# Kernel tuning notes

Measured on AMD Instinct MI355X. Metric: run time of the kernel, lower is better.

Reference implementation:

```python
import jax, jax.numpy as jnp
import numpy as np

N_NODES = 200000
N_EDGES = 6400000
D_IN, D_HID, D_OUT = 128, 16, 172


def gcn_conv(x, edge_index, W, b, n):
    """PyG GCNConv: add self-loops, symmetric D^-1/2 A D^-1/2 normalization,
    linear projection, scatter-add aggregation, bias."""
    src, dst = edge_index[0], edge_index[1]
    loops = jnp.arange(n, dtype=edge_index.dtype)
    src = jnp.concatenate([src, loops])
    dst = jnp.concatenate([dst, loops])
    # in-degree with self-loops (>= 1, so rsqrt is safe)
    deg = jax.ops.segment_sum(jnp.ones_like(dst, dtype=x.dtype), dst, num_segments=n)
    dinv = jax.lax.rsqrt(deg)
    lin = x @ W  # [n, d_out]
    norm = dinv[src] * dinv[dst]  # per-edge normalization
    msg = lin[src] * norm[:, None]  # gather + scale
    out = jax.ops.segment_sum(msg, dst, num_segments=n)  # scatter-add
    return out + b


def setup_inputs() -> dict:
    key = jax.random.key(0)
    k1, k2, k3, k4, k5, k6 = jax.random.split(key, 6)
    x = jax.random.normal(k1, (N_NODES, D_IN), dtype=jnp.float32)
    edge_index = jax.random.randint(k2, (2, N_EDGES), 0, N_NODES, dtype=jnp.int64)
    W1 = jax.random.normal(k3, (D_IN, D_HID), dtype=jnp.float32) * (1.0 / np.sqrt(D_IN))
    b1 = jnp.zeros((D_HID,), dtype=jnp.float32)
    W2 = jax.random.normal(k4, (D_HID, D_OUT), dtype=jnp.float32) * (1.0 / np.sqrt(D_HID))
    b2 = jnp.zeros((D_OUT,), dtype=jnp.float32)
    return {"x": x, "edge_index": edge_index, "W1": W1, "b1": b1, "W2": W2, "b2": b2}


def reference(x, edge_index, W1, b1, W2, b2):
    n = x.shape[0]
    # CRD: GCNConv -> relu (dropout is identity in eval mode)
    h = jax.nn.relu(gcn_conv(x, edge_index, W1, b1, n))
    # CLS: GCNConv -> log_softmax over classes
    logits = gcn_conv(h, edge_index, W2, b2, n)
    return jax.nn.log_softmax(logits, axis=1)
```

## Files before the change

kernel.cpp:

```cpp
#include <hip/hip_runtime.h>
#include <hip/hip_fp16.h>

#define N_NODES 200000
#define N_EDGES 6400000
#define D_IN    128
#define D_HID   16
#define D_OUT   172

#define NS1     800
#define EPB     8000
#define SBN     782
#define SB_NODES 256

#define O_BTOT  0
#define O_BASE  1024
#define O_CNT1  2048
#define O_COL   2048
#define O_ROW   6402048
#define O_DINV  6602112
#define O_PACK  6802112
#define O_F16A  6802112
#define O_F16B  8402112
#define O_AGG2  10002112

__global__ __launch_bounds__(256) void k_hist1(const int* __restrict__ dst,
                                               unsigned* __restrict__ counts) {
    __shared__ unsigned cnt[SBN];
    for (int i = threadIdx.x; i < SBN; i += 256) cnt[i] = 0;
    __syncthreads();
    const int* dp = dst + blockIdx.x * EPB;
    for (int i = threadIdx.x; i < EPB; i += 256)
        atomicAdd(&cnt[dp[i] >> 8], 1u);
    __syncthreads();
    unsigned* out = counts + (size_t)blockIdx.x * SBN;
    for (int i = threadIdx.x; i < SBN; i += 256) out[i] = cnt[i];
}

__global__ __launch_bounds__(256) void k_scan_col(unsigned* __restrict__ counts,
                                                  unsigned* __restrict__ btot) {
    __shared__ unsigned arr[NS1];
    int b = blockIdx.x;
    for (int i = threadIdx.x; i < NS1; i += 256)
        arr[i] = counts[(size_t)i * SBN + b];
    __syncthreads();
    if (threadIdx.x < 64) {
        int l = threadIdx.x;
        int lo = l * 13, hi = min(lo + 13, NS1);
        unsigned sum = 0;
        for (int i = lo; i < hi; ++i) sum += arr[i];
        unsigned incl = sum;
#pragma unroll
        for (int o = 1; o < 64; o <<= 1) {
            unsigned tmp = __shfl_up(incl, o);
            if (l >= o) incl += tmp;
        }
        if (l == 63) btot[b] = incl;
        unsigned run = incl - sum;
        for (int i = lo; i < hi; ++i) { unsigned v = arr[i]; arr[i] = run; run += v; }
    }
    __syncthreads();
    for (int i = threadIdx.x; i < NS1; i += 256)
        counts[(size_t)i * SBN + b] = arr[i];
}

__global__ __launch_bounds__(64) void k_scan_base(const unsigned* __restrict__ btot,
                                                  unsigned* __restrict__ base) {
    int l = threadIdx.x;
    int lo = l * 13, hi = min(lo + 13, SBN);
    unsigned sum = 0;
    for (int i = lo; i < hi; ++i) sum += btot[i];
    unsigned incl = sum;
#pragma unroll
    for (int o = 1; o < 64; o <<= 1) {
        unsigned tmp = __shfl_up(incl, o);
        if (l >= o) incl += tmp;
    }
    unsigned run = incl - sum;
    for (int i = lo; i < hi; ++i) { unsigned v = btot[i]; base[i] = run; run += v; }
    if (l == 63) base[SBN] = incl;
}

__global__ __launch_bounds__(256) void k_scatter1(const int* __restrict__ src,
                                                  const int* __restrict__ dst,
                                                  const unsigned* __restrict__ counts,
                                                  const unsigned* __restrict__ base,
                                                  unsigned* __restrict__ packed) {
    __shared__ unsigned off[SBN];
    const unsigned* crow = counts + (size_t)blockIdx.x * SBN;
    for (int i = threadIdx.x; i < SBN; i += 256) off[i] = base[i] + crow[i];
    __syncthreads();
    const int* sp = src + blockIdx.x * EPB;
    const int* dp = dst + blockIdx.x * EPB;
    for (int i = threadIdx.x; i < EPB; i += 256) {
        int s = sp[i], d = dp[i];
        unsigned slot = atomicAdd(&off[d >> 8], 1u);
        packed[slot] = ((unsigned)(d & (SB_NODES - 1)) << 18) | (unsigned)s;
    }
}

__global__ __launch_bounds__(256) void k_csr(const unsigned* __restrict__ packed,
                                             const unsigned* __restrict__ base,
                                             int* __restrict__ rowptr,
                                             float* __restrict__ dinv,
                                             int* __restrict__ col) {
    __shared__ unsigned cnt[SB_NODES];
    __shared__ unsigned off[SB_NODES];
    __shared__ unsigned wsum[4];
    int t = threadIdx.x, sb = blockIdx.x;
    unsigned beg = base[sb], end = base[sb + 1];
    cnt[t] = 0;
    __syncthreads();
    for (unsigned i = beg + t; i < end; i += 256)
        atomicAdd(&cnt[packed[i] >> 18], 1u);
    __syncthreads();
    unsigned e = cnt[t];
    int lane = t & 63, wid = t >> 6;
    unsigned incl = e;
#pragma unroll
    for (int o = 1; o < 64; o <<= 1) {
        unsigned tmp = __shfl_up(incl, o);
        if (lane >= o) incl += tmp;
    }
    if (lane == 63) wsum[wid] = incl;
    __syncthreads();
    unsigned wbase = 0;
    for (int w = 0; w < wid; ++w) wbase += wsum[w];
    unsigned ex = wbase + incl - e;
    off[t] = ex;
    int n0 = sb * SB_NODES + t;
    if (n0 <= N_NODES) rowptr[n0] = (int)(beg + ex);
    if (n0 <  N_NODES) dinv[n0]   = rsqrtf((float)(e + 1));
    __syncthreads();
    for (unsigned i = beg + t; i < end; i += 256) {
        unsigned p = packed[i];
        unsigned slot = atomicAdd(&off[p >> 18], 1u);
        col[beg + slot] = (int)(p & 0x3FFFFu);
    }
}

__global__ __launch_bounds__(256) void k_lin1(const float* __restrict__ x,
                                              const float* __restrict__ W1,
                                              const float* __restrict__ dinv,
                                              __half* __restrict__ lin) {
    __shared__ float sW[D_IN * D_HID];
    for (int t = threadIdx.x; t < D_IN * D_HID; t += 256) sW[t] = W1[t];
    __syncthreads();

    int g  = threadIdx.x & 3;
    int nl = threadIdx.x >> 2;
    int n  = blockIdx.x * 64 + nl;

    float acc[16];
#pragma unroll
    for (int j = 0; j < 16; ++j) acc[j] = 0.f;

    const float4* xr = (const float4*)(x + (size_t)n * D_IN + g * 32);
#pragma unroll
    for (int i = 0; i < 8; ++i) {
        float4 xv = xr[i];
        int k = g * 32 + i * 4;
#pragma unroll
        for (int j = 0; j < 16; ++j) {
            acc[j] += xv.x * sW[(k + 0) * 16 + j] + xv.y * sW[(k + 1) * 16 + j]
                    + xv.z * sW[(k + 2) * 16 + j] + xv.w * sW[(k + 3) * 16 + j];
        }
    }
#pragma unroll
    for (int j = 0; j < 16; ++j) {
        acc[j] += __shfl_xor(acc[j], 1);
        acc[j] += __shfl_xor(acc[j], 2);
    }
    float di = dinv[n];
    ushort4 pk;
    pk.x = __half_as_ushort(__float2half(acc[g * 4 + 0] * di));
    pk.y = __half_as_ushort(__float2half(acc[g * 4 + 1] * di));
    pk.z = __half_as_ushort(__float2half(acc[g * 4 + 2] * di));
    pk.w = __half_as_ushort(__float2half(acc[g * 4 + 3] * di));
    *(ushort4*)(lin + (size_t)n * 16 + g * 4) = pk;
}

template <int MODE>
__global__ __launch_bounds__(256) void k_gather(const int* __restrict__ rowptr,
                                                const int* __restrict__ col,
                                                const float* __restrict__ dinv,
                                                const __half* __restrict__ fin,
                                                const float* __restrict__ bias,
                                                void* __restrict__ outv) {
    int t = threadIdx.x;
    int n = blockIdx.x * 16 + (t >> 4);
    int lane = t & 15;
    int beg = rowptr[n], end = rowptr[n + 1];
    float a0 = __half2float(fin[n * 16 + lane]);
    float a1 = 0.f, a2 = 0.f, a3 = 0.f, a4 = 0.f, a5 = 0.f, a6 = 0.f, a7 = 0.f;
    int i = beg;
    for (; i + 8 <= end; i += 8) {
        int s0 = col[i + 0], s1 = col[i + 1], s2 = col[i + 2], s3 = col[i + 3];
        int s4 = col[i + 4], s5 = col[i + 5], s6 = col[i + 6], s7 = col[i + 7];
        float f0 = __half2float(fin[s0 * 16 + lane]);
        float f1 = __half2float(fin[s1 * 16 + lane]);
        float f2 = __half2float(fin[s2 * 16 + lane]);
        float f3 = __half2float(fin[s3 * 16 + lane]);
        float f4 = __half2float(fin[s4 * 16 + lane]);
        float f5 = __half2float(fin[s5 * 16 + lane]);
        float f6 = __half2float(fin[s6 * 16 + lane]);
        float f7 = __half2float(fin[s7 * 16 + lane]);
        a0 += f0; a1 += f1; a2 += f2; a3 += f3;
        a4 += f4; a5 += f5; a6 += f6; a7 += f7;
    }
    for (; i < end; ++i) a0 += __half2float(fin[col[i] * 16 + lane]);
    float acc = ((a0 + a1) + (a2 + a3)) + ((a4 + a5) + (a6 + a7));
    float dd = dinv[n];
    float v = acc * dd;
    if (MODE) {
        v = fmaxf(v + bias[lane], 0.f) * dd;
        ((__half*)outv)[n * 16 + lane] = __float2half(v);
    } else {
        ((float*)outv)[n * 16 + lane] = v;
    }
}

__global__ __launch_bounds__(256) void k_out(const float* __restrict__ agg2,
                                             const float* __restrict__ W2,
                                             const float* __restrict__ b2,
                                             float* __restrict__ out) {
    __shared__ float sWt[D_OUT * D_HID];
    __shared__ float sb[D_OUT];
    __shared__ float sl[64 * D_OUT];
    __shared__ float sls[64];
    int t = threadIdx.x;
    for (int m = t; m < D_OUT * D_HID; m += 256)
        sWt[m] = W2[(m & 15) * D_OUT + (m >> 4)];
    for (int m = t; m < D_OUT; m += 256) sb[m] = b2[m];
    __syncthreads();

    int nl = t >> 2, q = t & 3;
    int n  = blockIdx.x * 64 + nl;
    const float4* ar = (const float4*)(agg2 + (size_t)n * 16);
    float4 a0 = ar[0], a1 = ar[1], a2 = ar[2], a3 = ar[3];
    float a[16] = {a0.x, a0.y, a0.z, a0.w, a1.x, a1.y, a1.z, a1.w,
                   a2.x, a2.y, a2.z, a2.w, a3.x, a3.y, a3.z, a3.w};

    float mloc = -INFINITY;
    float* srow = sl + nl * D_OUT;
#pragma unroll 4
    for (int i = 0; i < 43; ++i) {
        int c = q + 4 * i;
        const float4* wr = (const float4*)(sWt + c * 16);
        float4 w0 = wr[0], w1 = wr[1], w2 = wr[2], w3 = wr[3];
        float l = sb[c];
        l += a[0]  * w0.x + a[1]  * w0.y + a[2]  * w0.z + a[3]  * w0.w;
        l += a[4]  * w1.x + a[5]  * w1.y + a[6]  * w1.z + a[7]  * w1.w;
        l += a[8]  * w2.x + a[9]  * w2.y + a[10] * w2.z + a[11] * w2.w;
        l += a[12] * w3.x + a[13] * w3.y + a[14] * w3.z + a[15] * w3.w;
        srow[c] = l;
        mloc = fmaxf(mloc, l);
    }
    mloc = fmaxf(mloc, __shfl_xor(mloc, 1));
    mloc = fmaxf(mloc, __shfl_xor(mloc, 2));
    float sloc = 0.f;
#pragma unroll 4
    for (int i = 0; i < 43; ++i) sloc += __expf(srow[q + 4 * i] - mloc);
    sloc += __shfl_xor(sloc, 1);
    sloc += __shfl_xor(sloc, 2);
    if (q == 0) sls[nl] = mloc + __logf(sloc);
    __syncthreads();

    const float4* sl4 = (const float4*)sl;
    float4* ob = (float4*)(out + (size_t)blockIdx.x * 64 * D_OUT);
    for (int jj = t; jj < 64 * D_OUT / 4; jj += 256) {
        float4 v = sl4[jj];
        float ls = sls[jj / 43];
        v.x -= ls; v.y -= ls; v.z -= ls; v.w -= ls;
        ob[jj] = v;
    }
}

extern "C" void kernel_launch(void* const* d_in, const int* in_sizes, int n_in,
                              void* d_out, int out_size, void* d_ws, size_t ws_size,
                              hipStream_t stream) {
    const float* x     = (const float*)d_in[0];
    const int*   edges = (const int*)d_in[1];
    const float* W1    = (const float*)d_in[2];
    const float* b1    = (const float*)d_in[3];
    const float* W2    = (const float*)d_in[4];
    const float* b2    = (const float*)d_in[5];
    float*       out   = (float*)d_out;

    const int* src = edges;
    const int* dst = edges + N_EDGES;

    unsigned* ws     = (unsigned*)d_ws;
    unsigned* btot   = ws + O_BTOT;
    unsigned* base   = ws + O_BASE;
    unsigned* counts = ws + O_CNT1;
    int*      col    = (int*)(ws + O_COL);
    int*      rowptr = (int*)(ws + O_ROW);
    float*    dinv   = (float*)(ws + O_DINV);
    unsigned* packed = ws + O_PACK;
    __half*   f16a   = (__half*)(ws + O_F16A);
    __half*   f16b   = (__half*)(ws + O_F16B);
    float*    agg2   = (float*)(ws + O_AGG2);

    k_hist1    <<<NS1, 256, 0, stream>>>(dst, counts);
    k_scan_col <<<SBN, 256, 0, stream>>>(counts, btot);
    k_scan_base<<<1,    64, 0, stream>>>(btot, base);
    k_scatter1 <<<NS1, 256, 0, stream>>>(src, dst, counts, base, packed);
    k_csr      <<<SBN, 256, 0, stream>>>(packed, base, rowptr, dinv, col);

    k_lin1     <<<N_NODES / 64, 256, 0, stream>>>(x, W1, dinv, f16a);
    k_gather<1><<<N_NODES / 16, 256, 0, stream>>>(rowptr, col, dinv, f16a, b1, f16b);

    k_gather<0><<<N_NODES / 16, 256, 0, stream>>>(rowptr, col, dinv, f16b, b1, agg2);
    k_out      <<<N_NODES / 64, 256, 0, stream>>>(agg2, W2, b2, out);
}
```

Before: 487.9 us.

## Quantize gathered node features to int8 and stage scatter through LDS

Adds per-tensor absmax tracking and an int8 quantization pass so both neighbor-aggregation gathers read 1-byte features with integer accumulation instead of fp16, halving random gather traffic. The scatter into coarse buckets is also restaged in shared memory with a local prefix sum so global writes are contiguous per bucket. This adds two quantize kernels and atomics, and int8 with a single global scale loses considerable precision, which risks tolerance failures.

```diff
diff --git a/kernel.cpp b/kernel.cpp
--- a/kernel.cpp
+++ b/kernel.cpp
@@ -14,14 +14,17 @@
 
 #define O_BTOT  0
 #define O_BASE  1024
-#define O_CNT1  2048
-#define O_COL   2048
-#define O_ROW   6402048
-#define O_DINV  6602112
-#define O_PACK  6802112
-#define O_F16A  6802112
-#define O_F16B  8402112
-#define O_AGG2  10002112
+#define O_SMAX  2048
+#define O_CNT1  2112
+#define O_COL   2112
+#define O_ROW   6402112
+#define O_DINV  6602176
+#define O_PACK  6802176
+#define O_F16A  6802176
+#define O_Q8A   8402176
+#define O_F16B  9202176
+#define O_Q8B   10802176
+#define O_AGG2  6802176
 
 __global__ __launch_bounds__(256) void k_hist1(const int* __restrict__ dst,
                                                unsigned* __restrict__ counts) {
@@ -64,8 +67,10 @@
 }
 
 __global__ __launch_bounds__(64) void k_scan_base(const unsigned* __restrict__ btot,
-                                                  unsigned* __restrict__ base) {
+                                                  unsigned* __restrict__ base,
+                                                  unsigned* __restrict__ smax) {
     int l = threadIdx.x;
+    if (l < 2) smax[l] = 0;
     int lo = l * 13, hi = min(lo + 13, SBN);
     unsigned sum = 0;
     for (int i = lo; i < hi; ++i) sum += btot[i];
@@ -85,16 +90,55 @@
                                                   const unsigned* __restrict__ counts,
                                                   const unsigned* __restrict__ base,
                                                   unsigned* __restrict__ packed) {
+    __shared__ unsigned       sdat[EPB];
+    __shared__ unsigned short sbkt[EPB];
+    __shared__ unsigned cnt[SBN];
     __shared__ unsigned off[SBN];
+    __shared__ unsigned gbs[SBN];
+    __shared__ unsigned wsum[4];
+    int t = threadIdx.x;
     const unsigned* crow = counts + (size_t)blockIdx.x * SBN;
-    for (int i = threadIdx.x; i < SBN; i += 256) off[i] = base[i] + crow[i];
+    for (int i = t; i < SBN; i += 256) { cnt[i] = 0; gbs[i] = base[i] + crow[i]; }
     __syncthreads();
     const int* sp = src + blockIdx.x * EPB;
     const int* dp = dst + blockIdx.x * EPB;
-    for (int i = threadIdx.x; i < EPB; i += 256) {
+    for (int i = t; i < EPB; i += 256) atomicAdd(&cnt[dp[i] >> 8], 1u);
+    __syncthreads();
+    int lane = t & 63, wid = t >> 6;
+    int b0 = t * 4;
+    unsigned c0v = (b0 + 0 < SBN) ? cnt[b0 + 0] : 0;
+    unsigned c1v = (b0 + 1 < SBN) ? cnt[b0 + 1] : 0;
+    unsigned c2v = (b0 + 2 < SBN) ? cnt[b0 + 2] : 0;
+    unsigned c3v = (b0 + 3 < SBN) ? cnt[b0 + 3] : 0;
+    unsigned mysum = c0v + c1v + c2v + c3v;
+    unsigned incl = mysum;
+#pragma unroll
+    for (int o = 1; o < 64; o <<= 1) {
+        unsigned tmp = __shfl_up(incl, o);
+        if (lane >= o) incl += tmp;
+    }
+    if (lane == 63) wsum[wid] = incl;
+    __syncthreads();
+    unsigned wbase = 0;
+    for (int w = 0; w < wid; ++w) wbase += wsum[w];
+    unsigned run = wbase + incl - mysum;
+    if (b0 + 0 < SBN) { off[b0 + 0] = run; run += c0v; }
+    if (b0 + 1 < SBN) { off[b0 + 1] = run; run += c1v; }
+    if (b0 + 2 < SBN) { off[b0 + 2] = run; run += c2v; }
+    if (b0 + 3 < SBN) { off[b0 + 3] = run; run += c3v; }
+    __syncthreads();
+    for (int i = t; i < EPB; i += 256) {
         int s = sp[i], d = dp[i];
-        unsigned slot = atomicAdd(&off[d >> 8], 1u);
-        packed[slot] = ((unsigned)(d & (SB_NODES - 1)) << 18) | (unsigned)s;
+        unsigned b = (unsigned)d >> 8;
+        unsigned slot = atomicAdd(&off[b], 1u);
+        sdat[slot] = ((unsigned)(d & (SB_NODES - 1)) << 18) | (unsigned)s;
+        sbkt[slot] = (unsigned short)b;
+    }
+    __syncthreads();
+    for (int i = t; i < EPB; i += 256) {
+        unsigned b = sbkt[i];
+        unsigned start = off[b] - cnt[b];
+        packed[gbs[b] + (i - start)] = sdat[i];
     }
 }
 
@@ -141,8 +185,11 @@
 __global__ __launch_bounds__(256) void k_lin1(const float* __restrict__ x,
                                               const float* __restrict__ W1,
                                               const float* __restrict__ dinv,
-                                              __half* __restrict__ lin) {
+                                              __half* __restrict__ lin,
+                                              unsigned* __restrict__ smax0) {
     __shared__ float sW[D_IN * D_HID];
+    __shared__ unsigned lmax;
+    if (threadIdx.x == 0) lmax = 0;
     for (int t = threadIdx.x; t < D_IN * D_HID; t += 256) sW[t] = W1[t];
     __syncthreads();
 
@@ -171,49 +218,79 @@
         acc[j] += __shfl_xor(acc[j], 2);
     }
     float di = dinv[n];
+    float v0 = acc[g * 4 + 0] * di, v1 = acc[g * 4 + 1] * di;
+    float v2 = acc[g * 4 + 2] * di, v3 = acc[g * 4 + 3] * di;
     ushort4 pk;
-    pk.x = __half_as_ushort(__float2half(acc[g * 4 + 0] * di));
-    pk.y = __half_as_ushort(__float2half(acc[g * 4 + 1] * di));
-    pk.z = __half_as_ushort(__float2half(acc[g * 4 + 2] * di));
-    pk.w = __half_as_ushort(__float2half(acc[g * 4 + 3] * di));
+    pk.x = __half_as_ushort(__float2half(v0));
+    pk.y = __half_as_ushort(__float2half(v1));
+    pk.z = __half_as_ushort(__float2half(v2));
+    pk.w = __half_as_ushort(__float2half(v3));
     *(ushort4*)(lin + (size_t)n * 16 + g * 4) = pk;
+    float m = fmaxf(fmaxf(fabsf(v0), fabsf(v1)), fmaxf(fabsf(v2), fabsf(v3)));
+    atomicMax(&lmax, __float_as_uint(m));
+    __syncthreads();
+    if (threadIdx.x == 0) atomicMax(smax0, lmax);
+}
+
+__global__ __launch_bounds__(256) void k_quant(const __half2* __restrict__ hin,
+                                               const unsigned* __restrict__ smax,
+                                               uchar4* __restrict__ q8) {
+    int i = blockIdx.x * 256 + threadIdx.x;
+    float mx = __uint_as_float(*smax);
+    float rs = mx > 0.f ? 127.0f / mx : 0.f;
+    __half2 p0 = hin[2 * i], p1 = hin[2 * i + 1];
+    float2 f0 = __half22float2(p0), f1 = __half22float2(p1);
+    int q0 = min(max(__float2int_rn(f0.x * rs), -127), 127);
+    int q1 = min(max(__float2int_rn(f0.y * rs), -127), 127);
+    int q2 = min(max(__float2int_rn(f1.x * rs), -127), 127);
+    int q3 = min(max(__float2int_rn(f1.y * rs), -127), 127);
+    uchar4 o;
+    o.x = (unsigned char)q0; o.y = (unsigned char)q1;
+    o.z = (unsigned char)q2; o.w = (unsigned char)q3;
+    q8[i] = o;
 }
 
 template <int MODE>
-__global__ __launch_bounds__(256) void k_gather(const int* __restrict__ rowptr,
-                                                const int* __restrict__ col,
-                                                const float* __restrict__ dinv,
-                                                const __half* __restrict__ fin,
-                                                const float* __restrict__ bias,
-                                                void* __restrict__ outv) {
+__global__ __launch_bounds__(256) void k_gather8(const int* __restrict__ rowptr,
+                                                 const int* __restrict__ col,
+                                                 const float* __restrict__ dinv,
+                                                 const signed char* __restrict__ q8,
+                                                 const unsigned* __restrict__ sin,
+                                                 unsigned* __restrict__ sout,
+                                                 const float* __restrict__ bias,
+                                                 void* __restrict__ outv) {
+    __shared__ unsigned lmax;
     int t = threadIdx.x;
+    if (MODE) {
+        if (t == 0) lmax = 0;
+        __syncthreads();
+    }
     int n = blockIdx.x * 16 + (t >> 4);
     int lane = t & 15;
     int beg = rowptr[n], end = rowptr[n + 1];
-    float a0 = __half2float(fin[n * 16 + lane]);
-    float a1 = 0.f, a2 = 0.f, a3 = 0.f, a4 = 0.f, a5 = 0.f, a6 = 0.f, a7 = 0.f;
+    int a0 = q8[n * 16 + lane];
+    int a1 = 0, a2 = 0, a3 = 0, a4 = 0, a5 = 0, a6 = 0, a7 = 0;
     int i = beg;
     for (; i + 8 <= end; i += 8) {
         int s0 = col[i + 0], s1 = col[i + 1], s2 = col[i + 2], s3 = col[i + 3];
         int s4 = col[i + 4], s5 = col[i + 5], s6 = col[i + 6], s7 = col[i + 7];
-        float f0 = __half2float(fin[s0 * 16 + lane]);
-        float f1 = __half2float(fin[s1 * 16 + lane]);
-        float f2 = __half2float(fin[s2 * 16 + lane]);
-        float f3 = __half2float(fin[s3 * 16 + lane]);
-        float f4 = __half2float(fin[s4 * 16 + lane]);
-        float f5 = __half2float(fin[s5 * 16 + lane]);
-        float f6 = __half2float(fin[s6 * 16 + lane]);
-        float f7 = __half2float(fin[s7 * 16 + lane]);
-        a0 += f0; a1 += f1; a2 += f2; a3 += f3;
-        a4 += f4; a5 += f5; a6 += f6; a7 += f7;
-    }
-    for (; i < end; ++i) a0 += __half2float(fin[col[i] * 16 + lane]);
-    float acc = ((a0 + a1) + (a2 + a3)) + ((a4 + a5) + (a6 + a7));
+        int b0 = q8[s0 * 16 + lane], b1v = q8[s1 * 16 + lane];
+        int b2 = q8[s2 * 16 + lane], b3 = q8[s3 * 16 + lane];
+        int b4 = q8[s4 * 16 + lane], b5 = q8[s5 * 16 + lane];
+        int b6 = q8[s6 * 16 + lane], b7 = q8[s7 * 16 + lane];
+        a0 += b0; a1 += b1v; a2 += b2; a3 += b3;
+        a4 += b4; a5 += b5; a6 += b6; a7 += b7;
+    }
+    for (; i < end; ++i) a0 += q8[col[i] * 16 + lane];
+    int isum = ((a0 + a1) + (a2 + a3)) + ((a4 + a5) + (a6 + a7));
     float dd = dinv[n];
-    float v = acc * dd;
+    float v = (float)isum * (__uint_as_float(*sin) * (1.0f / 127.0f)) * dd;
     if (MODE) {
         v = fmaxf(v + bias[lane], 0.f) * dd;
         ((__half*)outv)[n * 16 + lane] = __float2half(v);
+        atomicMax(&lmax, __float_as_uint(v));
+        __syncthreads();
+        if (t == 0) atomicMax(sout, lmax);
     } else {
         ((float*)outv)[n * 16 + lane] = v;
     }
@@ -292,24 +369,30 @@
     unsigned* ws     = (unsigned*)d_ws;
     unsigned* btot   = ws + O_BTOT;
     unsigned* base   = ws + O_BASE;
+    unsigned* smax   = ws + O_SMAX;
     unsigned* counts = ws + O_CNT1;
     int*      col    = (int*)(ws + O_COL);
     int*      rowptr = (int*)(ws + O_ROW);
     float*    dinv   = (float*)(ws + O_DINV);
     unsigned* packed = ws + O_PACK;
     __half*   f16a   = (__half*)(ws + O_F16A);
+    signed char* q8a = (signed char*)(ws + O_Q8A);
     __half*   f16b   = (__half*)(ws + O_F16B);
+    signed char* q8b = (signed char*)(ws + O_Q8B);
     float*    agg2   = (float*)(ws + O_AGG2);
 
     k_hist1    <<<NS1, 256, 0, stream>>>(dst, counts);
     k_scan_col <<<SBN, 256, 0, stream>>>(counts, btot);
-    k_scan_base<<<1,    64, 0, stream>>>(btot, base);
+    k_scan_base<<<1,    64, 0, stream>>>(btot, base, smax);
     k_scatter1 <<<NS1, 256, 0, stream>>>(src, dst, counts, base, packed);
     k_csr      <<<SBN, 256, 0, stream>>>(packed, base, rowptr, dinv, col);
 
-    k_lin1     <<<N_NODES / 64, 256, 0, stream>>>(x, W1, dinv, f16a);
-    k_gather<1><<<N_NODES / 16, 256, 0, stream>>>(rowptr, col, dinv, f16a, b1, f16b);
-
-    k_gather<0><<<N_NODES / 16, 256, 0, stream>>>(rowptr, col, dinv, f16b, b1, agg2);
+    k_lin1     <<<N_NODES / 64, 256, 0, stream>>>(x, W1, dinv, f16a, smax);
+    k_quant    <<<3125, 256, 0, stream>>>((const __half2*)f16a, smax, (uchar4*)q8a);
+    k_gather8<1><<<N_NODES / 16, 256, 0, stream>>>(rowptr, col, dinv, q8a,
+                                                   smax, smax + 1, b1, f16b);
+    k_quant    <<<3125, 256, 0, stream>>>((const __half2*)f16b, smax + 1, (uchar4*)q8b);
+    k_gather8<0><<<N_NODES / 16, 256, 0, stream>>>(rowptr, col, dinv, q8b,
+                                                   smax + 1, nullptr, b1, agg2);
     k_out      <<<N_NODES / 64, 256, 0, stream>>>(agg2, W2, b2, out);
 }
```

New measurement: 519.9 us. +6.6%, slower.

## Stage scatter through LDS for coalesced writes; gather half2 per lane

Applied to the files above, without the earlier changes.

The edge scatter kernel now counts and prefix-sums bucket sizes locally, places packed edges into shared memory sorted by bucket, then writes each bucket's run to global memory as contiguous runs. This replaces random scattered global stores with mostly contiguous ones. It costs a second local pass and about 48KB of LDS per block, which may lower occupancy. Separately, the gather kernels have each lane load a half2, so 8 lanes cover a 16-wide row and each block handles 32 nodes. That halves the threads per node and gives wider loads.

```diff
diff --git a/kernel.cpp b/kernel.cpp
--- a/kernel.cpp
+++ b/kernel.cpp
@@ -85,16 +85,55 @@
                                                   const unsigned* __restrict__ counts,
                                                   const unsigned* __restrict__ base,
                                                   unsigned* __restrict__ packed) {
+    __shared__ unsigned       sdat[EPB];
+    __shared__ unsigned short sbkt[EPB];
+    __shared__ unsigned cnt[SBN];
     __shared__ unsigned off[SBN];
+    __shared__ unsigned gbs[SBN];
+    __shared__ unsigned wsum[4];
+    int t = threadIdx.x;
     const unsigned* crow = counts + (size_t)blockIdx.x * SBN;
-    for (int i = threadIdx.x; i < SBN; i += 256) off[i] = base[i] + crow[i];
+    for (int i = t; i < SBN; i += 256) { cnt[i] = 0; gbs[i] = base[i] + crow[i]; }
     __syncthreads();
     const int* sp = src + blockIdx.x * EPB;
     const int* dp = dst + blockIdx.x * EPB;
-    for (int i = threadIdx.x; i < EPB; i += 256) {
+    for (int i = t; i < EPB; i += 256) atomicAdd(&cnt[dp[i] >> 8], 1u);
+    __syncthreads();
+    int lane = t & 63, wid = t >> 6;
+    int b0 = t * 4;
+    unsigned c0v = (b0 + 0 < SBN) ? cnt[b0 + 0] : 0;
+    unsigned c1v = (b0 + 1 < SBN) ? cnt[b0 + 1] : 0;
+    unsigned c2v = (b0 + 2 < SBN) ? cnt[b0 + 2] : 0;
+    unsigned c3v = (b0 + 3 < SBN) ? cnt[b0 + 3] : 0;
+    unsigned mysum = c0v + c1v + c2v + c3v;
+    unsigned incl = mysum;
+#pragma unroll
+    for (int o = 1; o < 64; o <<= 1) {
+        unsigned tmp = __shfl_up(incl, o);
+        if (lane >= o) incl += tmp;
+    }
+    if (lane == 63) wsum[wid] = incl;
+    __syncthreads();
+    unsigned wbase = 0;
+    for (int w = 0; w < wid; ++w) wbase += wsum[w];
+    unsigned run = wbase + incl - mysum;
+    if (b0 + 0 < SBN) { off[b0 + 0] = run; run += c0v; }
+    if (b0 + 1 < SBN) { off[b0 + 1] = run; run += c1v; }
+    if (b0 + 2 < SBN) { off[b0 + 2] = run; run += c2v; }
+    if (b0 + 3 < SBN) { off[b0 + 3] = run; run += c3v; }
+    __syncthreads();
+    for (int i = t; i < EPB; i += 256) {
         int s = sp[i], d = dp[i];
-        unsigned slot = atomicAdd(&off[d >> 8], 1u);
-        packed[slot] = ((unsigned)(d & (SB_NODES - 1)) << 18) | (unsigned)s;
+        unsigned b = (unsigned)d >> 8;
+        unsigned slot = atomicAdd(&off[b], 1u);
+        sdat[slot] = ((unsigned)(d & (SB_NODES - 1)) << 18) | (unsigned)s;
+        sbkt[slot] = (unsigned short)b;
+    }
+    __syncthreads();
+    for (int i = t; i < EPB; i += 256) {
+        unsigned b = sbkt[i];
+        unsigned start = off[b] - cnt[b];
+        packed[gbs[b] + (i - start)] = sdat[i];
     }
 }
 
@@ -183,39 +222,48 @@
 __global__ __launch_bounds__(256) void k_gather(const int* __restrict__ rowptr,
                                                 const int* __restrict__ col,
                                                 const float* __restrict__ dinv,
-                                                const __half* __restrict__ fin,
+                                                const __half2* __restrict__ fin,
                                                 const float* __restrict__ bias,
                                                 void* __restrict__ outv) {
     int t = threadIdx.x;
-    int n = blockIdx.x * 16 + (t >> 4);
-    int lane = t & 15;
+    int n = blockIdx.x * 32 + (t >> 3);
+    int lane = t & 7;
     int beg = rowptr[n], end = rowptr[n + 1];
-    float a0 = __half2float(fin[n * 16 + lane]);
-    float a1 = 0.f, a2 = 0.f, a3 = 0.f, a4 = 0.f, a5 = 0.f, a6 = 0.f, a7 = 0.f;
+    float2 a0 = __half22float2(fin[n * 8 + lane]);
+    float2 a1 = {0,0}, a2 = {0,0}, a3 = {0,0};
+    float2 a4 = {0,0}, a5 = {0,0}, a6 = {0,0}, a7 = {0,0};
     int i = beg;
     for (; i + 8 <= end; i += 8) {
         int s0 = col[i + 0], s1 = col[i + 1], s2 = col[i + 2], s3 = col[i + 3];
         int s4 = col[i + 4], s5 = col[i + 5], s6 = col[i + 6], s7 = col[i + 7];
-        float f0 = __half2float(fin[s0 * 16 + lane]);
-        float f1 = __half2float(fin[s1 * 16 + lane]);
-        float f2 = __half2float(fin[s2 * 16 + lane]);
-        float f3 = __half2float(fin[s3 * 16 + lane]);
-        float f4 = __half2float(fin[s4 * 16 + lane]);
-        float f5 = __half2float(fin[s5 * 16 + lane]);
-        float f6 = __half2float(fin[s6 * 16 + lane]);
-        float f7 = __half2float(fin[s7 * 16 + lane]);
-        a0 += f0; a1 += f1; a2 += f2; a3 += f3;
-        a4 += f4; a5 += f5; a6 += f6; a7 += f7;
-    }
-    for (; i < end; ++i) a0 += __half2float(fin[col[i] * 16 + lane]);
-    float acc = ((a0 + a1) + (a2 + a3)) + ((a4 + a5) + (a6 + a7));
+        __half2 h0 = fin[s0 * 8 + lane], h1 = fin[s1 * 8 + lane];
+        __half2 h2 = fin[s2 * 8 + lane], h3 = fin[s3 * 8 + lane];
+        __half2 h4 = fin[s4 * 8 + lane], h5 = fin[s5 * 8 + lane];
+        __half2 h6 = fin[s6 * 8 + lane], h7 = fin[s7 * 8 + lane];
+        float2 f0 = __half22float2(h0), f1 = __half22float2(h1);
+        float2 f2 = __half22float2(h2), f3 = __half22float2(h3);
+        float2 f4 = __half22float2(h4), f5 = __half22float2(h5);
+        float2 f6 = __half22float2(h6), f7 = __half22float2(h7);
+        a0.x += f0.x; a0.y += f0.y;  a1.x += f1.x; a1.y += f1.y;
+        a2.x += f2.x; a2.y += f2.y;  a3.x += f3.x; a3.y += f3.y;
+        a4.x += f4.x; a4.y += f4.y;  a5.x += f5.x; a5.y += f5.y;
+        a6.x += f6.x; a6.y += f6.y;  a7.x += f7.x; a7.y += f7.y;
+    }
+    for (; i < end; ++i) {
+        float2 f = __half22float2(fin[col[i] * 8 + lane]);
+        a0.x += f.x; a0.y += f.y;
+    }
+    float vx = ((a0.x + a1.x) + (a2.x + a3.x)) + ((a4.x + a5.x) + (a6.x + a7.x));
+    float vy = ((a0.y + a1.y) + (a2.y + a3.y)) + ((a4.y + a5.y) + (a6.y + a7.y));
     float dd = dinv[n];
-    float v = acc * dd;
+    vx *= dd; vy *= dd;
     if (MODE) {
-        v = fmaxf(v + bias[lane], 0.f) * dd;
-        ((__half*)outv)[n * 16 + lane] = __float2half(v);
+        float2 b2v = ((const float2*)bias)[lane];
+        vx = fmaxf(vx + b2v.x, 0.f) * dd;
+        vy = fmaxf(vy + b2v.y, 0.f) * dd;
+        ((__half2*)outv)[n * 8 + lane] = __floats2half2_rn(vx, vy);
     } else {
-        ((float*)outv)[n * 16 + lane] = v;
+        ((float2*)outv)[n * 8 + lane] = make_float2(vx, vy);
     }
 }
 
@@ -308,8 +356,10 @@
     k_csr      <<<SBN, 256, 0, stream>>>(packed, base, rowptr, dinv, col);
 
     k_lin1     <<<N_NODES / 64, 256, 0, stream>>>(x, W1, dinv, f16a);
-    k_gather<1><<<N_NODES / 16, 256, 0, stream>>>(rowptr, col, dinv, f16a, b1, f16b);
-
-    k_gather<0><<<N_NODES / 16, 256, 0, stream>>>(rowptr, col, dinv, f16b, b1, agg2);
+    k_gather<1><<<N_NODES / 32, 256, 0, stream>>>(rowptr, col, dinv,
+                                                  (const __half2*)f16a, b1, f16b);
+
+    k_gather<0><<<N_NODES / 32, 256, 0, stream>>>(rowptr, col, dinv,
+                                                  (const __half2*)f16b, b1, agg2);
     k_out      <<<N_NODES / 64, 256, 0, stream>>>(agg2, W2, b2, out);
 }
```

New measurement: 425.9 us. -12.7%, faster.
